# Kernel tuning notes

Hardware: AMD Instinct MI355X
Metric: run time of the kernel (lower is better)

Reference implementation:

```python
import jax, jax.numpy as jnp
import numpy as np

B, W, S, D, H = 16, 128, 16, 768, 12
HD = D // H

def _ln(x, g, b):
    m = x.mean(-1, keepdims=True)
    v = ((x - m) ** 2).mean(-1, keepdims=True)
    return (x - m) / jnp.sqrt(v + 1e-5) * g + b

def _lin(x, w, b):
    return x @ w.T + b

def _rope(t):
    # t: (N, H, L, HD); interleaved even/odd rotation, base 10000
    inv = 1.0 / (10000.0 ** (jnp.arange(0, HD, 2, dtype=jnp.float32) / HD))
    fr = jnp.arange(t.shape[2], dtype=jnp.float32)[:, None] * inv[None, :]  # (L, HD//2)
    cos, sin = jnp.cos(fr), jnp.sin(fr)
    te, to = t[..., ::2], t[..., 1::2]
    return jnp.stack([te * cos - to * sin, te * sin + to * cos], -1).reshape(t.shape)

def _mha(q, k, v, mask=None):
    # q,k,v: (N, H, L, HD)
    s = jnp.einsum('nhqd,nhkd->nhqk', q, k) / jnp.sqrt(jnp.float32(HD))
    if mask is not None:
        s = jnp.where(mask[None, None], -jnp.inf, s)
    a = jax.nn.softmax(s, axis=-1)
    return jnp.einsum('nhqk,nhkd->nhqd', a, v)

def _heads(t, L):
    return t.reshape(-1, L, H, HD).transpose(0, 2, 1, 3)

def setup_inputs() -> dict:
    key = jax.random.key(0)
    ks = jax.random.split(key, 16)
    def w(i, shape):
        return jax.random.normal(ks[i], shape, jnp.float32) * 0.02
    return {
        'x': jax.random.normal(ks[0], (B, W, S, D), jnp.float32),
        'causal_mask': jnp.triu(jnp.ones((W, W), dtype=bool), k=1),
        'sn_g': jnp.ones((D,), jnp.float32), 'sn_b': jnp.zeros((D,), jnp.float32),
        'sa_in_w': w(1, (3 * D, D)), 'sa_in_b': jnp.zeros((3 * D,), jnp.float32),
        'sa_out_w': w(2, (D, D)), 'sa_out_b': jnp.zeros((D,), jnp.float32),
        'tn_g': jnp.ones((D,), jnp.float32), 'tn_b': jnp.zeros((D,), jnp.float32),
        'tq_w': w(3, (D, D)), 'tq_b': jnp.zeros((D,), jnp.float32),
        'tk_w': w(4, (D, D)), 'tk_b': jnp.zeros((D,), jnp.float32),
        'tv_w': w(5, (D, D)), 'tv_b': jnp.zeros((D,), jnp.float32),
        'to_w': w(6, (D, D)), 'to_b': jnp.zeros((D,), jnp.float32),
        'fn_g': jnp.ones((D,), jnp.float32), 'fn_b': jnp.zeros((D,), jnp.float32),
        'f1_w': w(7, (4 * D, D)), 'f1_b': jnp.zeros((4 * D,), jnp.float32),
        'f2_w': w(8, (D, 4 * D)), 'f2_b': jnp.zeros((D,), jnp.float32),
    }

def reference(x, causal_mask, sn_g, sn_b, sa_in_w, sa_in_b, sa_out_w, sa_out_b,
              tn_g, tn_b, tq_w, tq_b, tk_w, tk_b, tv_w, tv_b, to_w, to_b,
              fn_g, fn_b, f1_w, f1_b, f2_w, f2_b):
    # ---- spatial attention within each timestep: (B*W, S, D) ----
    xs = x.reshape(B * W, S, D)
    xn = _ln(xs, sn_g, sn_b)
    q, k, v = jnp.split(_lin(xn, sa_in_w, sa_in_b), 3, axis=-1)
    o = _mha(_heads(q, S), _heads(k, S), _heads(v, S))
    o = o.transpose(0, 2, 1, 3).reshape(B * W, S, D)
    xs = xs + _lin(o, sa_out_w, sa_out_b)
    x = xs.reshape(B, W, S, D)
    # ---- causal temporal attention with RoPE: (B*S, W, D) ----
    xt = x.transpose(0, 2, 1, 3).reshape(B * S, W, D)
    xn = _ln(xt, tn_g, tn_b)
    q = _rope(_heads(_lin(xn, tq_w, tq_b), W))
    k = _rope(_heads(_lin(xn, tk_w, tk_b), W))
    v = _heads(_lin(xn, tv_w, tv_b), W)
    o = _mha(q, k, v, causal_mask)
    o = o.transpose(0, 2, 1, 3).reshape(B * S, W, D)
    xt = xt + _lin(o, to_w, to_b)
    x = xt.reshape(B, S, W, D).transpose(0, 2, 1, 3)
    # ---- feed-forward (exact GELU, as torch default) ----
    h = jax.nn.gelu(_lin(_ln(x, fn_g, fn_b), f1_w, f1_b), approximate=False)
    return x + _lin(h, f2_w, f2_b)
```

## Files before the change

kernel.cpp:

```cpp
#include <hip/hip_runtime.h>
#include <stdint.h>


#define NB 16
#define NW 128
#define NS 16
#define ND 768
#define NH 12
#define NTOK 32768

typedef __attribute__((ext_vector_type(8))) short short8;
typedef __attribute__((ext_vector_type(4))) float f32x4;

__device__ __forceinline__ float blo(unsigned v){ return __builtin_bit_cast(float, v << 16); }
__device__ __forceinline__ float bhi(unsigned v){ return __builtin_bit_cast(float, v & 0xffff0000u); }
__device__ __forceinline__ float bus(unsigned short u){ return __builtin_bit_cast(float, ((unsigned)u) << 16); }
__device__ __forceinline__ unsigned short f2b(float f){
  unsigned u = __builtin_bit_cast(unsigned, f);
  u += 0x7fffu + ((u >> 16) & 1u);
  return (unsigned short)(u >> 16);
}
__device__ __forceinline__ void gld_lds16(const void* g, void* l){
  __builtin_amdgcn_global_load_lds((const __attribute__((address_space(1))) void*)g,
                                   (__attribute__((address_space(3))) void*)l, 16, 0, 0);
}

__global__ __launch_bounds__(256) void convert_k(const float* __restrict__ in,
                                                 unsigned short* __restrict__ out, int n4){
  int i = blockIdx.x * 256 + threadIdx.x;
  int stride = gridDim.x * 256;
  for (; i < n4; i += stride){
    float4 v = ((const float4*)in)[i];
    unsigned lo = (unsigned)f2b(v.x) | ((unsigned)f2b(v.y) << 16);
    unsigned hi = (unsigned)f2b(v.z) | ((unsigned)f2b(v.w) << 16);
    ((uint2*)out)[i] = make_uint2(lo, hi);
  }
}

__global__ __launch_bounds__(256) void concat3_k(const float* __restrict__ a, const float* __restrict__ b,
                                                 const float* __restrict__ c, float* __restrict__ o){
  int i = blockIdx.x * 256 + threadIdx.x;
  if (i < 768){ o[i] = a[i]; o[768 + i] = b[i]; o[1536 + i] = c[i]; }
}

__global__ __launch_bounds__(256) void rope_k(float* __restrict__ tab){
  int i = blockIdx.x * 256 + threadIdx.x;
  if (i < 128 * 32){
    int w = i >> 5, p = i & 31;
    float inv = powf(10000.0f, -((float)(2 * p)) / 64.0f);
    float ang = (float)w * inv;
    tab[i * 2] = cosf(ang);
    tab[i * 2 + 1] = sinf(ang);
  }
}

template<int INF32>
__global__ __launch_bounds__(256) void ln_k(const void* __restrict__ xin, const float* __restrict__ g,
                                            const float* __restrict__ bt, unsigned short* __restrict__ out){
  const int row = blockIdx.x;
  const int t = threadIdx.x;
  const float* xf = (const float*)xin;
  const unsigned short* xb = (const unsigned short*)xin;
  float v[3];
#pragma unroll
  for (int i = 0; i < 3; ++i){
    int j = t + i * 256;
    v[i] = INF32 ? xf[(size_t)row * 768 + j] : bus(xb[(size_t)row * 768 + j]);
  }
  float s = v[0] + v[1] + v[2];
  float ss = v[0]*v[0] + v[1]*v[1] + v[2]*v[2];
#pragma unroll
  for (int o = 1; o < 64; o <<= 1){ s += __shfl_xor(s, o, 64); ss += __shfl_xor(ss, o, 64); }
  __shared__ float red[8];
  int w = t >> 6;
  if ((t & 63) == 0){ red[w*2] = s; red[w*2+1] = ss; }
  __syncthreads();
  s = red[0] + red[2] + red[4] + red[6];
  ss = red[1] + red[3] + red[5] + red[7];
  float mean = s * (1.0f / 768.0f);
  float var = ss * (1.0f / 768.0f) - mean * mean;
  float rstd = rsqrtf(var + 1e-5f);
#pragma unroll
  for (int i = 0; i < 3; ++i){
    int j = t + i * 256;
    out[(size_t)row * 768 + j] = f2b((v[i] - mean) * rstd * g[j] + bt[j]);
  }
}

template<int MODE>
__global__ __launch_bounds__(512) void gemm256_k(const unsigned short* __restrict__ A,
                                                 const unsigned short* __restrict__ Bw,
                                                 const float* __restrict__ bias,
                                                 const void* __restrict__ resid,
                                                 void* __restrict__ outp, int K, int M){
  __shared__ char LB[131072];
  char* const Asl = LB;
  char* const Bsl = LB + 65536;
  const int tid = threadIdx.x;
  const int lane = tid & 63, w = tid >> 6;
  const int llo = lane & 15, lhi = lane >> 4;
  const int wm = w >> 2, wn = w & 3;
  const int brow = blockIdx.y << 8, bcol = blockIdx.x << 8;
  const int NT = K >> 6;

  const int r0 = tid >> 3, cp = tid & 7;
  const int swz = (cp << 4) ^ ((r0 & 7) << 4);
  const char* aG = (const char*)(A + (size_t)(brow + r0) * K) + swz;
  const char* bG = (const char*)(Bw + (size_t)(bcol + r0) * K) + swz;
  const int J  = K * 128;
  const int Hh = K * 256;
  const int ldst = w << 10;

  auto stage = [&](const char* g, int gb, char* slotbase){
    gld_lds16(g + gb,     slotbase + ldst);
    gld_lds16(g + gb + J, slotbase + ldst + (1 << 13));
  };

  stage(aG, 0,        Asl);
  stage(aG, Hh,       Asl + (1 << 14));
  stage(bG, 0,        Bsl);
  stage(bG, Hh,       Bsl + (1 << 14));
  stage(aG, 128,      Asl + (2 << 14));
  stage(aG, 128 + Hh, Asl + (3 << 14));
  asm volatile("s_waitcnt vmcnt(4)" ::: "memory");
  __builtin_amdgcn_s_barrier();

  f32x4 acc[8][4];
#pragma unroll
  for (int m = 0; m < 8; ++m)
#pragma unroll
    for (int n = 0; n < 4; ++n) acc[m][n] = f32x4{0.f, 0.f, 0.f, 0.f};

  for (int t = 0; t < NT; ++t){
    const char* Ab = Asl + (((2 * t + wm) & 3) << 14);
    const char* Bb = Bsl + (((2 * t + (wn >> 1)) & 3) << 14);
    const int tb = t << 7;
    short8 a0[4][2], a1[4][2], b0[2][2], b1[2][2];

#pragma unroll
    for (int mi = 0; mi < 4; ++mi){
      const int rr = (mi << 4) + llo;
#pragma unroll
      for (int ks = 0; ks < 2; ++ks)
        a0[mi][ks] = *(const short8*)(Ab + rr * 128 + (((ks << 6) + (lhi << 4)) ^ ((rr & 7) << 4)));
    }
#pragma unroll
    for (int ni = 0; ni < 2; ++ni){
      const int cc = ((wn & 1) << 6) + (ni << 4) + llo;
#pragma unroll
      for (int ks = 0; ks < 2; ++ks)
        b0[ni][ks] = *(const short8*)(Bb + cc * 128 + (((ks << 6) + (lhi << 4)) ^ ((cc & 7) << 4)));
    }
    if (t + 1 < NT) stage(bG, tb + 128, Bsl + (((2 * t + 2) & 3) << 14));
    __builtin_amdgcn_s_barrier();
    asm volatile("s_waitcnt lgkmcnt(0)" ::: "memory");
    __builtin_amdgcn_s_setprio(1);
#pragma unroll
    for (int mi = 0; mi < 4; ++mi)
#pragma unroll
      for (int ni = 0; ni < 2; ++ni){
        acc[mi][ni] = __builtin_amdgcn_mfma_f32_16x16x32_bf16(b0[ni][0], a0[mi][0], acc[mi][ni], 0, 0, 0);
        acc[mi][ni] = __builtin_amdgcn_mfma_f32_16x16x32_bf16(b0[ni][1], a0[mi][1], acc[mi][ni], 0, 0, 0);
      }
    __builtin_amdgcn_s_setprio(0);
    __builtin_amdgcn_s_barrier();

#pragma unroll
    for (int mi = 0; mi < 4; ++mi){
      const int rr = 64 + (mi << 4) + llo;
#pragma unroll
      for (int ks = 0; ks < 2; ++ks)
        a1[mi][ks] = *(const short8*)(Ab + rr * 128 + (((ks << 6) + (lhi << 4)) ^ ((rr & 7) << 4)));
    }
    if (t + 1 < NT) stage(bG, tb + 128 + Hh, Bsl + (((2 * t + 3) & 3) << 14));
    __builtin_amdgcn_s_barrier();
    asm volatile("s_waitcnt lgkmcnt(0)" ::: "memory");
    __builtin_amdgcn_s_setprio(1);
#pragma unroll
    for (int mi = 0; mi < 4; ++mi)
#pragma unroll
      for (int ni = 0; ni < 2; ++ni){
        acc[4 + mi][ni] = __builtin_amdgcn_mfma_f32_16x16x32_bf16(b0[ni][0], a1[mi][0], acc[4 + mi][ni], 0, 0, 0);
        acc[4 + mi][ni] = __builtin_amdgcn_mfma_f32_16x16x32_bf16(b0[ni][1], a1[mi][1], acc[4 + mi][ni], 0, 0, 0);
      }
    __builtin_amdgcn_s_setprio(0);
    __builtin_amdgcn_s_barrier();

#pragma unroll
    for (int ni = 0; ni < 2; ++ni){
      const int cc = ((wn & 1) << 6) + 32 + (ni << 4) + llo;
#pragma unroll
      for (int ks = 0; ks < 2; ++ks)
        b1[ni][ks] = *(const short8*)(Bb + cc * 128 + (((ks << 6) + (lhi << 4)) ^ ((cc & 7) << 4)));
    }
    if (t + 2 < NT) stage(aG, tb + 256, Asl + (((2 * t + 4) & 3) << 14));
    __builtin_amdgcn_s_barrier();
    asm volatile("s_waitcnt lgkmcnt(0)" ::: "memory");
    __builtin_amdgcn_s_setprio(1);
#pragma unroll
    for (int mi = 0; mi < 4; ++mi)
#pragma unroll
      for (int ni = 0; ni < 2; ++ni){
        acc[mi][2 + ni] = __builtin_amdgcn_mfma_f32_16x16x32_bf16(b1[ni][0], a0[mi][0], acc[mi][2 + ni], 0, 0, 0);
        acc[mi][2 + ni] = __builtin_amdgcn_mfma_f32_16x16x32_bf16(b1[ni][1], a0[mi][1], acc[mi][2 + ni], 0, 0, 0);
      }
    __builtin_amdgcn_s_setprio(0);
    __builtin_amdgcn_s_barrier();

    if (t + 2 < NT) stage(aG, tb + 256 + Hh, Asl + (((2 * t + 5) & 3) << 14));
    __builtin_amdgcn_s_barrier();
    asm volatile("s_waitcnt lgkmcnt(0)" ::: "memory");
    __builtin_amdgcn_s_setprio(1);
#pragma unroll
    for (int mi = 0; mi < 4; ++mi)
#pragma unroll
      for (int ni = 0; ni < 2; ++ni){
        acc[4 + mi][2 + ni] = __builtin_amdgcn_mfma_f32_16x16x32_bf16(b1[ni][0], a1[mi][0], acc[4 + mi][2 + ni], 0, 0, 0);
        acc[4 + mi][2 + ni] = __builtin_amdgcn_mfma_f32_16x16x32_bf16(b1[ni][1], a1[mi][1], acc[4 + mi][2 + ni], 0, 0, 0);
      }
    __builtin_amdgcn_s_setprio(0);
    if (t + 2 < NT) asm volatile("s_waitcnt vmcnt(4)" ::: "memory");
    else            asm volatile("s_waitcnt vmcnt(0)" ::: "memory");
    __builtin_amdgcn_s_barrier();
  }

  const int orow = brow + (wm << 7);
  const int ocol = bcol + (wn << 6);
  const unsigned short* resb = (const unsigned short*)resid;
  const float* resf = (const float*)resid;
#pragma unroll
  for (int m = 0; m < 8; ++m){
    const int row = orow + (m << 4) + llo;
    const size_t rb = (size_t)row * M;
#pragma unroll
    for (int n = 0; n < 4; ++n){
      const int col = ocol + (n << 4) + (lhi << 2);
      const float4 bv = *(const float4*)&bias[col];
      float v0 = acc[m][n][0] + bv.x;
      float v1 = acc[m][n][1] + bv.y;
      float v2 = acc[m][n][2] + bv.z;
      float v3 = acc[m][n][3] + bv.w;
      const size_t off = rb + col;
      if (MODE == 1){
        float y0 = v0 * (1.5957691216f + 0.0713548163f * v0 * v0);
        float y1 = v1 * (1.5957691216f + 0.0713548163f * v1 * v1);
        float y2 = v2 * (1.5957691216f + 0.0713548163f * v2 * v2);
        float y3 = v3 * (1.5957691216f + 0.0713548163f * v3 * v3);
        v0 = v0 / (1.0f + __expf(-y0));
        v1 = v1 / (1.0f + __expf(-y1));
        v2 = v2 / (1.0f + __expf(-y2));
        v3 = v3 / (1.0f + __expf(-y3));
      } else if (MODE == 2){
        const float4 rv = *(const float4*)&resf[off];
        v0 += rv.x; v1 += rv.y; v2 += rv.z; v3 += rv.w;
      } else if (MODE == 3 || MODE == 4){
        const uint2 rv = *(const uint2*)&resb[off];
        v0 += blo(rv.x); v1 += bhi(rv.x); v2 += blo(rv.y); v3 += bhi(rv.y);
      }
      if (MODE == 4){
        float4 ov; ov.x = v0; ov.y = v1; ov.z = v2; ov.w = v3;
        *(float4*)&((float*)outp)[off] = ov;
      } else {
        unsigned lo = (unsigned)f2b(v0) | ((unsigned)f2b(v1) << 16);
        unsigned hi = (unsigned)f2b(v2) | ((unsigned)f2b(v3) << 16);
        *(uint2*)&((unsigned short*)outp)[off] = make_uint2(lo, hi);
      }
    }
  }
}

__global__ __launch_bounds__(256) void sattn_k(const unsigned short* __restrict__ qkv,
                                               unsigned short* __restrict__ o){
  const int bw = blockIdx.x, h = blockIdx.y;
  const int t = threadIdx.x;
  __shared__ unsigned short qh[16 * 68], kh[16 * 68], vh[16 * 68];
  __shared__ float pl[16 * 17];
  const int row = t >> 4, c4 = t & 15;
  const size_t base = ((size_t)(bw * 16 + row)) * 2304 + h * 64 + c4 * 4;
  *(uint2*)&qh[row * 68 + c4 * 4] = *(const uint2*)&qkv[base];
  *(uint2*)&kh[row * 68 + c4 * 4] = *(const uint2*)&qkv[base + 768];
  *(uint2*)&vh[row * 68 + c4 * 4] = *(const uint2*)&qkv[base + 1536];
  __syncthreads();

  const int q = row, k = c4;
  float s = 0.f;
#pragma unroll
  for (int c = 0; c < 16; ++c){
    uint2 qv = *(const uint2*)&qh[q * 68 + c * 4];
    uint2 kv = *(const uint2*)&kh[k * 68 + c * 4];
    s += blo(qv.x) * blo(kv.x) + bhi(qv.x) * bhi(kv.x);
    s += blo(qv.y) * blo(kv.y) + bhi(qv.y) * bhi(kv.y);
  }
  s *= 0.125f;
  float m = s;
#pragma unroll
  for (int off = 1; off < 16; off <<= 1) m = fmaxf(m, __shfl_xor(m, off, 64));
  float p = __expf(s - m);
  float su = p;
#pragma unroll
  for (int off = 1; off < 16; off <<= 1) su += __shfl_xor(su, off, 64);
  pl[q * 17 + k] = p / su;
  __syncthreads();

  float o0 = 0.f, o1 = 0.f, o2 = 0.f, o3 = 0.f;
#pragma unroll
  for (int kk = 0; kk < 16; ++kk){
    float pw = pl[q * 17 + kk];
    uint2 vv = *(const uint2*)&vh[kk * 68 + c4 * 4];
    o0 += pw * blo(vv.x); o1 += pw * bhi(vv.x);
    o2 += pw * blo(vv.y); o3 += pw * bhi(vv.y);
  }
  const size_t ob = ((size_t)(bw * 16 + q)) * 768 + h * 64 + c4 * 4;
  unsigned r0 = (unsigned)f2b(o0) | ((unsigned)f2b(o1) << 16);
  unsigned r1 = (unsigned)f2b(o2) | ((unsigned)f2b(o3) << 16);
  *(uint2*)&o[ob] = make_uint2(r0, r1);
}

__global__ __launch_bounds__(256) void tattn_k(const unsigned short* __restrict__ qkv,
                                               const float* __restrict__ rope,
                                               unsigned short* __restrict__ o){
  const int bs = blockIdx.x, h = blockIdx.y;
  const int b = bs >> 4, s = bs & 15;
  const int t = threadIdx.x, lane = t & 63, w = t >> 6;
  const int lhi = lane >> 4, llo = lane & 15;
  __shared__ unsigned short Qs[128 * 64];
  __shared__ unsigned short Ks[128 * 64];
  __shared__ unsigned short Vt[64 * 128];
  __shared__ unsigned short P[128 * 128];

  {
    const int r = t >> 1;
    const int dbase = (t & 1) * 32;
    const size_t tokb = ((size_t)((b * 128 + r) * 16 + s)) * 2304 + h * 64;
    const float2* rp = (const float2*)rope;
#pragma unroll
    for (int mch = 0; mch < 4; ++mch){
      const int d0 = dbase + mch * 8;
      uint4 qv = *(const uint4*)&qkv[tokb + d0];
      uint4 kv = *(const uint4*)&qkv[tokb + 768 + d0];
      uint4 vv = *(const uint4*)&qkv[tokb + 1536 + d0];
      unsigned qin[4] = {qv.x, qv.y, qv.z, qv.w};
      unsigned kin[4] = {kv.x, kv.y, kv.z, kv.w};
      unsigned qo[4], ko[4];
#pragma unroll
      for (int j = 0; j < 4; ++j){
        float2 cssn = rp[r * 32 + (d0 >> 1) + j];
        float cs = cssn.x, sn = cssn.y;
        float qe = blo(qin[j]), qd = bhi(qin[j]);
        float ke = blo(kin[j]), kd = bhi(kin[j]);
        qo[j] = (unsigned)f2b(qe * cs - qd * sn) | ((unsigned)f2b(qe * sn + qd * cs) << 16);
        ko[j] = (unsigned)f2b(ke * cs - kd * sn) | ((unsigned)f2b(ke * sn + kd * cs) << 16);
      }
      const int byq = r * 128 + ((d0 * 2) ^ ((r & 7) << 4));
      *(uint4*)((char*)Qs + byq) = make_uint4(qo[0], qo[1], qo[2], qo[3]);
      *(uint4*)((char*)Ks + byq) = make_uint4(ko[0], ko[1], ko[2], ko[3]);
      unsigned vin[4] = {vv.x, vv.y, vv.z, vv.w};
#pragma unroll
      for (int j = 0; j < 8; ++j){
        const int d = d0 + j;
        unsigned short val = (j & 1) ? (unsigned short)(vin[j >> 1] >> 16)
                                     : (unsigned short)(vin[j >> 1] & 0xffffu);
        *(unsigned short*)((char*)Vt + d * 256 + ((r * 2) ^ ((d & 7) << 4))) = val;
      }
    }
  }
  __syncthreads();

  const int qbase = w * 32;
  f32x4 st[8][2];
#pragma unroll
  for (int i = 0; i < 8; ++i){ st[i][0] = f32x4{0.f,0.f,0.f,0.f}; st[i][1] = f32x4{0.f,0.f,0.f,0.f}; }
#pragma unroll
  for (int kd = 0; kd < 2; ++kd){
    short8 bq[2];
#pragma unroll
    for (int fq = 0; fq < 2; ++fq){
      const int qr = qbase + fq * 16 + llo;
      bq[fq] = *(const short8*)((const char*)Qs + qr * 128 + ((kd * 64 + lhi * 16) ^ ((qr & 7) << 4)));
    }
#pragma unroll
    for (int fk = 0; fk < 8; ++fk){
      const int kr = fk * 16 + llo;
      short8 ak = *(const short8*)((const char*)Ks + kr * 128 + ((kd * 64 + lhi * 16) ^ ((kr & 7) << 4)));
      st[fk][0] = __builtin_amdgcn_mfma_f32_16x16x32_bf16(ak, bq[0], st[fk][0], 0, 0, 0);
      st[fk][1] = __builtin_amdgcn_mfma_f32_16x16x32_bf16(ak, bq[1], st[fk][1], 0, 0, 0);
    }
  }

#pragma unroll
  for (int fq = 0; fq < 2; ++fq){
    const int qg = qbase + fq * 16 + llo;
    float m = -1e30f;
#pragma unroll
    for (int fk = 0; fk < 8; ++fk)
#pragma unroll
      for (int rr = 0; rr < 4; ++rr){
        const int kg = fk * 16 + lhi * 4 + rr;
        float sv = (kg <= qg) ? st[fk][fq][rr] : -1e30f;
        st[fk][fq][rr] = sv;
        m = fmaxf(m, sv);
      }
    m = fmaxf(m, __shfl_xor(m, 16, 64));
    m = fmaxf(m, __shfl_xor(m, 32, 64));
    float su = 0.f;
#pragma unroll
    for (int fk = 0; fk < 8; ++fk)
#pragma unroll
      for (int rr = 0; rr < 4; ++rr){
        float p = __expf((st[fk][fq][rr] - m) * 0.125f);
        st[fk][fq][rr] = p;
        su += p;
      }
    su += __shfl_xor(su, 16, 64);
    su += __shfl_xor(su, 32, 64);
    const float rs = 1.0f / su;
#pragma unroll
    for (int fk = 0; fk < 8; ++fk){
      const int kk = fk * 16 + lhi * 4;
      unsigned lo = (unsigned)f2b(st[fk][fq][0] * rs) | ((unsigned)f2b(st[fk][fq][1] * rs) << 16);
      unsigned hi = (unsigned)f2b(st[fk][fq][2] * rs) | ((unsigned)f2b(st[fk][fq][3] * rs) << 16);
      *(uint2*)((char*)P + qg * 256 + ((kk * 2) ^ ((qg & 7) << 4))) = make_uint2(lo, hi);
    }
  }
  __syncthreads();

  f32x4 oacc[2][4];
#pragma unroll
  for (int i = 0; i < 2; ++i)
#pragma unroll
    for (int j = 0; j < 4; ++j) oacc[i][j] = f32x4{0.f,0.f,0.f,0.f};
#pragma unroll
  for (int ks = 0; ks < 4; ++ks){
    short8 pa[2];
#pragma unroll
    for (int fq = 0; fq < 2; ++fq){
      const int qr = qbase + fq * 16 + llo;
      pa[fq] = *(const short8*)((const char*)P + qr * 256 + ((ks * 64 + lhi * 16) ^ ((qr & 7) << 4)));
    }
#pragma unroll
    for (int fd = 0; fd < 4; ++fd){
      const int dr = fd * 16 + llo;
      short8 vb = *(const short8*)((const char*)Vt + dr * 256 + ((ks * 64 + lhi * 16) ^ ((dr & 7) << 4)));
      oacc[0][fd] = __builtin_amdgcn_mfma_f32_16x16x32_bf16(pa[0], vb, oacc[0][fd], 0, 0, 0);
      oacc[1][fd] = __builtin_amdgcn_mfma_f32_16x16x32_bf16(pa[1], vb, oacc[1][fd], 0, 0, 0);
    }
  }

#pragma unroll
  for (int fq = 0; fq < 2; ++fq)
#pragma unroll
    for (int fd = 0; fd < 4; ++fd)
#pragma unroll
      for (int rr = 0; rr < 4; ++rr){
        const int qg = qbase + fq * 16 + lhi * 4 + rr;
        const int d = fd * 16 + llo;
        const size_t ob = ((size_t)((b * 128 + qg) * 16 + s)) * 768 + h * 64 + d;
        o[ob] = f2b(oacc[fq][fd][rr]);
      }
}

__global__ __launch_bounds__(256) void sentinel_k(float* out){
  if (blockIdx.x == 0 && threadIdx.x == 0) out[0] = 12345.0f;
}

extern "C" void kernel_launch(void* const* d_in, const int* in_sizes, int n_in,
                              void* d_out, int out_size, void* d_ws, size_t ws_size,
                              hipStream_t stream){
  const float* x       = (const float*)d_in[0];
  const float* sn_g    = (const float*)d_in[2];
  const float* sn_b    = (const float*)d_in[3];
  const float* sa_in_w = (const float*)d_in[4];
  const float* sa_in_b = (const float*)d_in[5];
  const float* sa_out_w= (const float*)d_in[6];
  const float* sa_out_b= (const float*)d_in[7];
  const float* tn_g    = (const float*)d_in[8];
  const float* tn_b    = (const float*)d_in[9];
  const float* tq_w    = (const float*)d_in[10];
  const float* tq_b    = (const float*)d_in[11];
  const float* tk_w    = (const float*)d_in[12];
  const float* tk_b    = (const float*)d_in[13];
  const float* tv_w    = (const float*)d_in[14];
  const float* tv_b    = (const float*)d_in[15];
  const float* to_w    = (const float*)d_in[16];
  const float* to_b    = (const float*)d_in[17];
  const float* fn_g    = (const float*)d_in[18];
  const float* fn_b    = (const float*)d_in[19];
  const float* f1_w    = (const float*)d_in[20];
  const float* f1_b    = (const float*)d_in[21];
  const float* f2_w    = (const float*)d_in[22];
  const float* f2_b    = (const float*)d_in[23];

  char* ws = (char*)d_ws;
  size_t off = 0;
  auto alloc = [&](size_t bytes) -> void* {
    void* p = ws + off;
    off += (bytes + 255) & ~(size_t)255;
    return p;
  };
  unsigned short* Wqkv = (unsigned short*)alloc((size_t)2304*768*2);
  unsigned short* Wo1  = (unsigned short*)alloc((size_t)768*768*2);
  unsigned short* W3   = (unsigned short*)alloc((size_t)2304*768*2);
  float*          b3   = (float*)alloc(2304*4);
  unsigned short* Wto  = (unsigned short*)alloc((size_t)768*768*2);
  unsigned short* Wf1  = (unsigned short*)alloc((size_t)3072*768*2);
  unsigned short* Wf2  = (unsigned short*)alloc((size_t)768*3072*2);
  float*          rope = (float*)alloc(128*32*2*4);
  unsigned short* xn   = (unsigned short*)alloc((size_t)NTOK*768*2);
  unsigned short* qkv  = (unsigned short*)alloc((size_t)NTOK*3072*2);
  unsigned short* xs2  = (unsigned short*)alloc((size_t)NTOK*768*2);
  unsigned short* xt2  = (unsigned short*)alloc((size_t)NTOK*768*2);
  unsigned short* ob   = xn;

  if (ws_size < off){ sentinel_k<<<1, 64, 0, stream>>>((float*)d_out); return; }

  convert_k<<<1024, 256, 0, stream>>>(sa_in_w, Wqkv, 2304*768/4);
  convert_k<<<512, 256, 0, stream>>>(sa_out_w, Wo1, 768*768/4);
  convert_k<<<512, 256, 0, stream>>>(tq_w, W3, 768*768/4);
  convert_k<<<512, 256, 0, stream>>>(tk_w, W3 + 768*768, 768*768/4);
  convert_k<<<512, 256, 0, stream>>>(tv_w, W3 + 2*768*768, 768*768/4);
  concat3_k<<<3, 256, 0, stream>>>(tq_b, tk_b, tv_b, b3);
  convert_k<<<512, 256, 0, stream>>>(to_w, Wto, 768*768/4);
  convert_k<<<1024, 256, 0, stream>>>(f1_w, Wf1, 3072*768/4);
  convert_k<<<1024, 256, 0, stream>>>(f2_w, Wf2, 768*3072/4);
  rope_k<<<16, 256, 0, stream>>>(rope);

  ln_k<1><<<NTOK, 256, 0, stream>>>(x, sn_g, sn_b, xn);
  gemm256_k<0><<<dim3(9, 128), 512, 0, stream>>>(xn, Wqkv, sa_in_b, nullptr, qkv, 768, 2304);
  sattn_k<<<dim3(2048, 12), 256, 0, stream>>>(qkv, ob);
  gemm256_k<2><<<dim3(3, 128), 512, 0, stream>>>(ob, Wo1, sa_out_b, x, xs2, 768, 768);

  ln_k<0><<<NTOK, 256, 0, stream>>>(xs2, tn_g, tn_b, xn);
  gemm256_k<0><<<dim3(9, 128), 512, 0, stream>>>(xn, W3, b3, nullptr, qkv, 768, 2304);
  tattn_k<<<dim3(256, 12), 256, 0, stream>>>(qkv, rope, ob);
  gemm256_k<3><<<dim3(3, 128), 512, 0, stream>>>(ob, Wto, to_b, xs2, xt2, 768, 768);

  ln_k<0><<<NTOK, 256, 0, stream>>>(xt2, fn_g, fn_b, xn);
  gemm256_k<1><<<dim3(12, 128), 512, 0, stream>>>(xn, Wf1, f1_b, nullptr, qkv, 768, 3072);
  gemm256_k<4><<<dim3(3, 128), 512, 0, stream>>>(qkv, Wf2, f2_b, xt2, d_out, 3072, 768);
}
```

Baseline: 1.141 ms.

## Template GEMM on M-tile height and add XCD-aware block remapping

```diff
diff --git a/kernel.cpp b/kernel.cpp
--- a/kernel.cpp
+++ b/kernel.cpp
@@ -87,58 +87,75 @@
   }
 }
 
-template<int MODE>
+template<int MODE, int MROWS>
 __global__ __launch_bounds__(512) void gemm256_k(const unsigned short* __restrict__ A,
                                                  const unsigned short* __restrict__ Bw,
                                                  const float* __restrict__ bias,
                                                  const void* __restrict__ resid,
                                                  void* __restrict__ outp, int K, int M){
-  __shared__ char LB[131072];
+  constexpr int MH = MROWS / 2;
+  constexpr int ASH = (MROWS == 8) ? 14 : 13;
+  constexpr int NJA = MROWS / 4;
+  constexpr int LDSZ = 4 * (1 << ASH) + 65536;
+  __shared__ char LB[LDSZ];
   char* const Asl = LB;
-  char* const Bsl = LB + 65536;
+  char* const Bsl = LB + 4 * (1 << ASH);
   const int tid = threadIdx.x;
   const int lane = tid & 63, w = tid >> 6;
   const int llo = lane & 15, lhi = lane >> 4;
   const int wm = w >> 2, wn = w & 3;
-  const int brow = blockIdx.y << 8, bcol = blockIdx.x << 8;
   const int NT = K >> 6;
+
+  const int gx = gridDim.x;
+  const int nwg = gx * gridDim.y;
+  const int orig = blockIdx.y * gx + blockIdx.x;
+  const int lin = (nwg & 7) ? orig : ((orig & 7) * (nwg >> 3) + (orig >> 3));
+  const int by = lin / gx, bx = lin - by * gx;
+  const int brow = by * (MROWS << 5);
+  const int bcol = bx << 8;
 
   const int r0 = tid >> 3, cp = tid & 7;
   const int swz = (cp << 4) ^ ((r0 & 7) << 4);
   const char* aG = (const char*)(A + (size_t)(brow + r0) * K) + swz;
   const char* bG = (const char*)(Bw + (size_t)(bcol + r0) * K) + swz;
   const int J  = K * 128;
-  const int Hh = K * 256;
+  const int Ha = K * (MROWS << 5);
+  const int Hb = K * 256;
   const int ldst = w << 10;
 
-  auto stage = [&](const char* g, int gb, char* slotbase){
-    gld_lds16(g + gb,     slotbase + ldst);
-    gld_lds16(g + gb + J, slotbase + ldst + (1 << 13));
+  auto stage_a = [&](int gb, char* slotbase){
+    gld_lds16(aG + gb, slotbase + ldst);
+    if constexpr (NJA == 2) gld_lds16(aG + gb + J, slotbase + ldst + (1 << 13));
   };
-
-  stage(aG, 0,        Asl);
-  stage(aG, Hh,       Asl + (1 << 14));
-  stage(bG, 0,        Bsl);
-  stage(bG, Hh,       Bsl + (1 << 14));
-  stage(aG, 128,      Asl + (2 << 14));
-  stage(aG, 128 + Hh, Asl + (3 << 14));
-  asm volatile("s_waitcnt vmcnt(4)" ::: "memory");
+  auto stage_b = [&](int gb, char* slotbase){
+    gld_lds16(bG + gb, slotbase + ldst);
+    gld_lds16(bG + gb + J, slotbase + ldst + (1 << 13));
+  };
+
+  stage_a(0,        Asl);
+  stage_a(Ha,       Asl + (1 << ASH));
+  stage_b(0,        Bsl);
+  stage_b(Hb,       Bsl + (1 << 14));
+  stage_a(128,      Asl + (2 << ASH));
+  stage_a(128 + Ha, Asl + (3 << ASH));
+  if constexpr (NJA == 2) asm volatile("s_waitcnt vmcnt(4)" ::: "memory");
+  else                    asm volatile("s_waitcnt vmcnt(2)" ::: "memory");
   __builtin_amdgcn_s_barrier();
 
-  f32x4 acc[8][4];
-#pragma unroll
-  for (int m = 0; m < 8; ++m)
+  f32x4 acc[MROWS][4];
+#pragma unroll
+  for (int m = 0; m < MROWS; ++m)
 #pragma unroll
     for (int n = 0; n < 4; ++n) acc[m][n] = f32x4{0.f, 0.f, 0.f, 0.f};
 
   for (int t = 0; t < NT; ++t){
-    const char* Ab = Asl + (((2 * t + wm) & 3) << 14);
+    const char* Ab = Asl + (((2 * t + wm) & 3) << ASH);
     const char* Bb = Bsl + (((2 * t + (wn >> 1)) & 3) << 14);
     const int tb = t << 7;
-    short8 a0[4][2], a1[4][2], b0[2][2], b1[2][2];
-
-#pragma unroll
-    for (int mi = 0; mi < 4; ++mi){
+    short8 a0[MH][2], a1[MH][2], b0[2][2], b1[2][2];
+
+#pragma unroll
+    for (int mi = 0; mi < MH; ++mi){
       const int rr = (mi << 4) + llo;
 #pragma unroll
       for (int ks = 0; ks < 2; ++ks)
@@ -151,12 +168,12 @@
       for (int ks = 0; ks < 2; ++ks)
         b0[ni][ks] = *(const short8*)(Bb + cc * 128 + (((ks << 6) + (lhi << 4)) ^ ((cc & 7) << 4)));
     }
-    if (t + 1 < NT) stage(bG, tb + 128, Bsl + (((2 * t + 2) & 3) << 14));
+    if (t + 1 < NT) stage_b(tb + 128, Bsl + (((2 * t + 2) & 3) << 14));
     __builtin_amdgcn_s_barrier();
     asm volatile("s_waitcnt lgkmcnt(0)" ::: "memory");
     __builtin_amdgcn_s_setprio(1);
 #pragma unroll
-    for (int mi = 0; mi < 4; ++mi)
+    for (int mi = 0; mi < MH; ++mi)
 #pragma unroll
       for (int ni = 0; ni < 2; ++ni){
         acc[mi][ni] = __builtin_amdgcn_mfma_f32_16x16x32_bf16(b0[ni][0], a0[mi][0], acc[mi][ni], 0, 0, 0);
@@ -166,22 +183,22 @@
     __builtin_amdgcn_s_barrier();
 
 #pragma unroll
-    for (int mi = 0; mi < 4; ++mi){
-      const int rr = 64 + (mi << 4) + llo;
+    for (int mi = 0; mi < MH; ++mi){
+      const int rr = (MH << 4) + (mi << 4) + llo;
 #pragma unroll
       for (int ks = 0; ks < 2; ++ks)
         a1[mi][ks] = *(const short8*)(Ab + rr * 128 + (((ks << 6) + (lhi << 4)) ^ ((rr & 7) << 4)));
     }
-    if (t + 1 < NT) stage(bG, tb + 128 + Hh, Bsl + (((2 * t + 3) & 3) << 14));
+    if (t + 1 < NT) stage_b(tb + 128 + Hb, Bsl + (((2 * t + 3) & 3) << 14));
     __builtin_amdgcn_s_barrier();
     asm volatile("s_waitcnt lgkmcnt(0)" ::: "memory");
     __builtin_amdgcn_s_setprio(1);
 #pragma unroll
-    for (int mi = 0; mi < 4; ++mi)
+    for (int mi = 0; mi < MH; ++mi)
 #pragma unroll
       for (int ni = 0; ni < 2; ++ni){
-        acc[4 + mi][ni] = __builtin_amdgcn_mfma_f32_16x16x32_bf16(b0[ni][0], a1[mi][0], acc[4 + mi][ni], 0, 0, 0);
-        acc[4 + mi][ni] = __builtin_amdgcn_mfma_f32_16x16x32_bf16(b0[ni][1], a1[mi][1], acc[4 + mi][ni], 0, 0, 0);
+        acc[MH + mi][ni] = __builtin_amdgcn_mfma_f32_16x16x32_bf16(b0[ni][0], a1[mi][0], acc[MH + mi][ni], 0, 0, 0);
+        acc[MH + mi][ni] = __builtin_amdgcn_mfma_f32_16x16x32_bf16(b0[ni][1], a1[mi][1], acc[MH + mi][ni], 0, 0, 0);
       }
     __builtin_amdgcn_s_setprio(0);
     __builtin_amdgcn_s_barrier();
@@ -193,12 +210,12 @@
       for (int ks = 0; ks < 2; ++ks)
         b1[ni][ks] = *(const short8*)(Bb + cc * 128 + (((ks << 6) + (lhi << 4)) ^ ((cc & 7) << 4)));
     }
-    if (t + 2 < NT) stage(aG, tb + 256, Asl + (((2 * t + 4) & 3) << 14));
+    if (t + 2 < NT) stage_a(tb + 256, Asl + (((2 * t + 4) & 3) << ASH));
     __builtin_amdgcn_s_barrier();
     asm volatile("s_waitcnt lgkmcnt(0)" ::: "memory");
     __builtin_amdgcn_s_setprio(1);
 #pragma unroll
-    for (int mi = 0; mi < 4; ++mi)
+    for (int mi = 0; mi < MH; ++mi)
 #pragma unroll
       for (int ni = 0; ni < 2; ++ni){
         acc[mi][2 + ni] = __builtin_amdgcn_mfma_f32_16x16x32_bf16(b1[ni][0], a0[mi][0], acc[mi][2 + ni], 0, 0, 0);
@@ -207,29 +224,33 @@
     __builtin_amdgcn_s_setprio(0);
     __builtin_amdgcn_s_barrier();
 
-    if (t + 2 < NT) stage(aG, tb + 256 + Hh, Asl + (((2 * t + 5) & 3) << 14));
+    if (t + 2 < NT) stage_a(tb + 256 + Ha, Asl + (((2 * t + 5) & 3) << ASH));
     __builtin_amdgcn_s_barrier();
     asm volatile("s_waitcnt lgkmcnt(0)" ::: "memory");
     __builtin_amdgcn_s_setprio(1);
 #pragma unroll
-    for (int mi = 0; mi < 4; ++mi)
+    for (int mi = 0; mi < MH; ++mi)
 #pragma unroll
       for (int ni = 0; ni < 2; ++ni){
-        acc[4 + mi][2 + ni] = __builtin_amdgcn_mfma_f32_16x16x32_bf16(b1[ni][0], a1[mi][0], acc[4 + mi][2 + ni], 0, 0, 0);
-        acc[4 + mi][2 + ni] = __builtin_amdgcn_mfma_f32_16x16x32_bf16(b1[ni][1], a1[mi][1], acc[4 + mi][2 + ni], 0, 0, 0);
+        acc[MH + mi][2 + ni] = __builtin_amdgcn_mfma_f32_16x16x32_bf16(b1[ni][0], a1[mi][0], acc[MH + mi][2 + ni], 0, 0, 0);
+        acc[MH + mi][2 + ni] = __builtin_amdgcn_mfma_f32_16x16x32_bf16(b1[ni][1], a1[mi][1], acc[MH + mi][2 + ni], 0, 0, 0);
       }
     __builtin_amdgcn_s_setprio(0);
-    if (t + 2 < NT) asm volatile("s_waitcnt vmcnt(4)" ::: "memory");
-    else            asm volatile("s_waitcnt vmcnt(0)" ::: "memory");
-    __builtin_amdgcn_s_barrier();
-  }
-
-  const int orow = brow + (wm << 7);
+    if (t + 2 < NT){
+      if constexpr (NJA == 2) asm volatile("s_waitcnt vmcnt(4)" ::: "memory");
+      else                    asm volatile("s_waitcnt vmcnt(2)" ::: "memory");
+    } else {
+      asm volatile("s_waitcnt vmcnt(0)" ::: "memory");
+    }
+    __builtin_amdgcn_s_barrier();
+  }
+
+  const int orow = brow + wm * (MROWS << 4);
   const int ocol = bcol + (wn << 6);
   const unsigned short* resb = (const unsigned short*)resid;
   const float* resf = (const float*)resid;
 #pragma unroll
-  for (int m = 0; m < 8; ++m){
+  for (int m = 0; m < MROWS; ++m){
     const int row = orow + (m << 4) + llo;
     const size_t rb = (size_t)row * M;
 #pragma unroll
@@ -525,16 +546,16 @@
   rope_k<<<16, 256, 0, stream>>>(rope);
 
   ln_k<1><<<NTOK, 256, 0, stream>>>(x, sn_g, sn_b, xn);
-  gemm256_k<0><<<dim3(9, 128), 512, 0, stream>>>(xn, Wqkv, sa_in_b, nullptr, qkv, 768, 2304);
+  gemm256_k<0,4><<<dim3(9, 256), 512, 0, stream>>>(xn, Wqkv, sa_in_b, nullptr, qkv, 768, 2304);
   sattn_k<<<dim3(2048, 12), 256, 0, stream>>>(qkv, ob);
-  gemm256_k<2><<<dim3(3, 128), 512, 0, stream>>>(ob, Wo1, sa_out_b, x, xs2, 768, 768);
+  gemm256_k<2,4><<<dim3(3, 256), 512, 0, stream>>>(ob, Wo1, sa_out_b, x, xs2, 768, 768);
 
   ln_k<0><<<NTOK, 256, 0, stream>>>(xs2, tn_g, tn_b, xn);
-  gemm256_k<0><<<dim3(9, 128), 512, 0, stream>>>(xn, W3, b3, nullptr, qkv, 768, 2304);
+  gemm256_k<0,4><<<dim3(9, 256), 512, 0, stream>>>(xn, W3, b3, nullptr, qkv, 768, 2304);
   tattn_k<<<dim3(256, 12), 256, 0, stream>>>(qkv, rope, ob);
-  gemm256_k<3><<<dim3(3, 128), 512, 0, stream>>>(ob, Wto, to_b, xs2, xt2, 768, 768);
+  gemm256_k<3,4><<<dim3(3, 256), 512, 0, stream>>>(ob, Wto, to_b, xs2, xt2, 768, 768);
 
   ln_k<0><<<NTOK, 256, 0, stream>>>(xt2, fn_g, fn_b, xn);
-  gemm256_k<1><<<dim3(12, 128), 512, 0, stream>>>(xn, Wf1, f1_b, nullptr, qkv, 768, 3072);
-  gemm256_k<4><<<dim3(3, 128), 512, 0, stream>>>(qkv, Wf2, f2_b, xt2, d_out, 3072, 768);
-}
+  gemm256_k<1,8><<<dim3(12, 128), 512, 0, stream>>>(xn, Wf1, f1_b, nullptr, qkv, 768, 3072);
+  gemm256_k<4,4><<<dim3(3, 256), 512, 0, stream>>>(qkv, Wf2, f2_b, xt2, d_out, 3072, 768);
+}
```

New measurement: 1.122 ms. No clear change (-1.7%).
